# Performance work log

Hardware: AMD Instinct MI355X
Metric: run time of the kernel (lower is better)

Reference implementation:

```python
import jax, jax.numpy as jnp
import numpy as np

N_NODES = 50000
N_EDGES = 1000000
N_EVAL = 100000
IN_DIM = 256
HID = 64
HEADS = 4
NEG_SLOPE = 0.2


def _glorot(key, shape):
    fan_in, fan_out = shape[0], shape[-1]
    lim = jnp.sqrt(6.0 / (fan_in + fan_out))
    return jax.random.uniform(key, shape, jnp.float32, -lim, lim)


def setup_inputs() -> dict:
    key = jax.random.key(0)
    ks = jax.random.split(key, 24)
    inp = {}
    inp["x"] = jax.random.normal(ks[0], (N_NODES, IN_DIM), jnp.float32)
    inp["edge_index"] = jax.random.randint(ks[1], (2, N_EDGES), 0, N_NODES, jnp.int64)
    inp["edge_src"] = jax.random.randint(ks[2], (N_EVAL,), 0, N_NODES, jnp.int64)
    inp["edge_dst"] = jax.random.randint(ks[3], (N_EVAL,), 0, N_NODES, jnp.int64)
    # encoder
    inp["enc_w"] = _glorot(ks[4], (IN_DIM, HID))
    inp["enc_b"] = jnp.zeros((HID,), jnp.float32)
    # GAT layer 1: HID -> HEADS*HID (concat)
    inp["gat1_w"] = _glorot(ks[5], (HID, HEADS * HID))
    inp["gat1_att_src"] = _glorot(ks[6], (HEADS, HID))
    inp["gat1_att_dst"] = _glorot(ks[7], (HEADS, HID))
    inp["gat1_b"] = jnp.zeros((HEADS * HID,), jnp.float32)
    # GAT layer 2: HEADS*HID -> HEADS*HID
    inp["gat2_w"] = _glorot(ks[8], (HEADS * HID, HEADS * HID))
    inp["gat2_att_src"] = _glorot(ks[9], (HEADS, HID))
    inp["gat2_att_dst"] = _glorot(ks[10], (HEADS, HID))
    inp["gat2_b"] = jnp.zeros((HEADS * HID,), jnp.float32)
    # link predictor MLP: 2*256 -> 64 -> 32 -> 1
    inp["lp1_w"] = _glorot(ks[11], (2 * HEADS * HID, HID))
    inp["lp1_b"] = jnp.zeros((HID,), jnp.float32)
    inp["lp2_w"] = _glorot(ks[12], (HID, HID // 2))
    inp["lp2_b"] = jnp.zeros((HID // 2,), jnp.float32)
    inp["lp3_w"] = _glorot(ks[13], (HID // 2, 1))
    inp["lp3_b"] = jnp.zeros((1,), jnp.float32)
    return inp


def gat_layer(x, src, dst, W, att_src, att_dst, bias, n_nodes):
    # x: [N, F_in] -> h: [N, H, C]
    h = (x @ W).reshape(n_nodes, HEADS, HID)
    a_s = jnp.einsum("nhc,hc->nh", h, att_src)  # per-node src logit part
    a_d = jnp.einsum("nhc,hc->nh", h, att_dst)  # per-node dst logit part
    e = jax.nn.leaky_relu(a_s[src] + a_d[dst], NEG_SLOPE)  # [E, H]
    # segment softmax over incoming edges of each dst node
    m = jax.ops.segment_max(e, dst, num_segments=n_nodes)  # [N, H]
    e = jnp.exp(e - m[dst])
    s = jax.ops.segment_sum(e, dst, num_segments=n_nodes)  # [N, H]
    alpha = e / (s[dst] + 1e-16)  # [E, H]
    msg = h[src] * alpha[:, :, None]  # [E, H, C]
    out = jax.ops.segment_sum(msg, dst, num_segments=n_nodes)  # [N, H, C]
    return out.reshape(n_nodes, HEADS * HID) + bias


def reference(x, edge_index, edge_src, edge_dst,
              enc_w, enc_b,
              gat1_w, gat1_att_src, gat1_att_dst, gat1_b,
              gat2_w, gat2_att_src, gat2_att_dst, gat2_b,
              lp1_w, lp1_b, lp2_w, lp2_b, lp3_w, lp3_b):
    n = x.shape[0]
    src, dst = edge_index[0], edge_index[1]
    # NodeEncoder
    h = jax.nn.relu(x @ enc_w + enc_b)
    # GAT layers (dropout is identity in eval)
    h = gat_layer(h, src, dst, gat1_w, gat1_att_src, gat1_att_dst, gat1_b, n)
    h = gat_layer(h, src, dst, gat2_w, gat2_att_src, gat2_att_dst, gat2_b, n)
    # link predictor on (src_feat, dst_feat) pairs
    pair = jnp.concatenate([h[edge_src], h[edge_dst]], axis=1)  # [Eval, 512]
    z = jax.nn.relu(pair @ lp1_w + lp1_b)
    z = jax.nn.relu(z @ lp2_w + lp2_b)
    scores = z @ lp3_w + lp3_b  # [Eval, 1]
    return scores
```

## Files before the change

kernel.cpp:

```cpp
#include <hip/hip_runtime.h>
#include <hip/hip_bf16.h>
#include <math.h>

#define NNODES 50000
#define HID    64
#define HEADS  4
#define FDIM   256

typedef __attribute__((ext_vector_type(8))) _Float16 half8v;
typedef __attribute__((ext_vector_type(4))) _Float16 half4v;
typedef __attribute__((ext_vector_type(4))) float f32x4;

__device__ __forceinline__ float lrelu(float x) { return fmaxf(x, 0.2f * x); }

__global__ void split_kernel(const float4* __restrict__ x, _Float16* __restrict__ xh, int n4)
{
  int t = blockIdx.x * blockDim.x + threadIdx.x;
  if (t >= n4) return;
  float4 v = x[t];
  half4v o = {(_Float16)v.x, (_Float16)v.y, (_Float16)v.z, (_Float16)v.w};
  *(half4v*)(xh + (size_t)t * 4) = o;
}

__global__ void wtconv_all_kernel(const float* __restrict__ enc_w, const float* __restrict__ g1_w,
                                  const float* __restrict__ g2_w, const float* __restrict__ lp1_w,
                                  _Float16* __restrict__ we, _Float16* __restrict__ w1,
                                  _Float16* __restrict__ w2, _Float16* __restrict__ wlp)
{
  int t = blockIdx.x * blockDim.x + threadIdx.x;
  float w; _Float16* dh; int di;
  if (t < 16384) {
    int n = t >> 8, k = t & 255;
    w = enc_w[(size_t)k * 64 + n]; dh = we; di = t;
  } else if (t < 32768) {
    int l = t - 16384; int n = l >> 6, k = l & 63;
    w = g1_w[(size_t)k * 256 + n]; dh = w1; di = l;
  } else if (t < 98304) {
    int l = t - 32768; int n = l >> 8, k = l & 255;
    w = g2_w[(size_t)k * 256 + n]; dh = w2; di = l;
  } else {
    int l = t - 98304; int n = l >> 8, k = l & 255;
    int srow = (n < 64) ? k : (256 + k);
    w = lp1_w[(size_t)srow * 64 + (n & 63)]; dh = wlp; di = l;
  }
  dh[di] = (_Float16)w;
}

__global__ void attcomb_kernel(const float* __restrict__ g1_w, const float* __restrict__ g1_as,
                               const float* __restrict__ g1_ad,
                               const float* __restrict__ g2_w, const float* __restrict__ g2_as,
                               const float* __restrict__ g2_ad,
                               _Float16* __restrict__ w1, _Float16* __restrict__ w2)
{
  int t = blockIdx.x * blockDim.x + threadIdx.x;
  if (t < 1024) {
    int j = t >> 6, k = t & 63;
    float v = 0.f;
    if (j < 8) {
      int head = j & 3;
      const float* att = (j < 4 ? g1_as : g1_ad) + head * 64;
      for (int c = 0; c < 64; ++c) v += g1_w[(size_t)k * 256 + head * 64 + c] * att[c];
    }
    w1[(256 + j) * 64 + k] = (_Float16)v;
  } else if (t < 5120) {
    int l = t - 1024; int j = l >> 8, k = l & 255;
    float v = 0.f;
    if (j < 8) {
      int head = j & 3;
      const float* att = (j < 4 ? g2_as : g2_ad) + head * 64;
      for (int c = 0; c < 64; ++c) v += g2_w[(size_t)k * 256 + head * 64 + c] * att[c];
    }
    w2[(256 + j) * 256 + k] = (_Float16)v;
  }
}

template<int KTOT, int NFRAG, int OUTMODE, bool LOGIT>
__global__ __launch_bounds__(256) void mfma_gemm(
    const _Float16* __restrict__ A, const _Float16* __restrict__ B,
    const float* __restrict__ bias,
    float* __restrict__ outF, _Float16* __restrict__ outH,
    float* __restrict__ a_s, float* __restrict__ a_d,
    int M, int Ntot)
{
  __shared__ _Float16 As[128 * 64];
  const int tid  = threadIdx.x;
  const int lane = tid & 63;
  const int wid  = tid >> 6;
  const int row0 = blockIdx.y * 128;
  const int col0 = blockIdx.x * 64;
  const bool lastblk = LOGIT && ((int)blockIdx.x == (int)gridDim.x - 1);

  f32x4 acc[2][NFRAG];
  f32x4 accL[2];
#pragma unroll
  for (int m = 0; m < 2; ++m) {
#pragma unroll
    for (int n = 0; n < NFRAG; ++n) acc[m][n] = (f32x4){0.f, 0.f, 0.f, 0.f};
    accL[m] = (f32x4){0.f, 0.f, 0.f, 0.f};
  }

  const int rsub = lane >> 3;
  const int slot = lane & 7;
  const int brow = col0 + (lane & 15);
  const int bk   = (lane >> 4) * 8;

  for (int kt = 0; kt < KTOT; kt += 64) {
#pragma unroll
    for (int i = 0; i < 4; ++i) {
      const int c  = i * 4 + wid;
      const int r  = c * 8 + rsub;
      const int gr = min(row0 + r, M - 1);
      const int ss = slot ^ rsub;
      const size_t goff = (size_t)gr * KTOT + kt + ss * 8;
      __builtin_amdgcn_global_load_lds(
          (const __attribute__((address_space(1))) void*)(A + goff),
          (__attribute__((address_space(3))) void*)(As + c * 512), 16, 0, 0);
    }
    __syncthreads();

#pragma unroll
    for (int ks = 0; ks < 2; ++ks) {
      half8v ah[2], bh[NFRAG];
#pragma unroll
      for (int mf = 0; mf < 2; ++mf) {
        const int r   = wid * 32 + mf * 16 + (lane & 15);
        const int sl  = (ks * 4 + (lane >> 4)) ^ (r & 7);
        ah[mf] = *(const half8v*)(As + r * 64 + sl * 8);
      }
#pragma unroll
      for (int nf = 0; nf < NFRAG; ++nf) {
        const size_t bo = (size_t)(brow + nf * 16) * KTOT + kt + ks * 32 + bk;
        bh[nf] = *(const half8v*)(B + bo);
      }
#pragma unroll
      for (int mf = 0; mf < 2; ++mf)
#pragma unroll
        for (int nf = 0; nf < NFRAG; ++nf)
          acc[mf][nf] = __builtin_amdgcn_mfma_f32_16x16x32_f16(ah[mf], bh[nf], acc[mf][nf], 0, 0, 0);
      if (lastblk) {
        const size_t bo = (size_t)(256 + (lane & 15)) * KTOT + kt + ks * 32 + bk;
        const half8v bhl = *(const half8v*)(B + bo);
#pragma unroll
        for (int mf = 0; mf < 2; ++mf)
          accL[mf] = __builtin_amdgcn_mfma_f32_16x16x32_f16(ah[mf], bhl, accL[mf], 0, 0, 0);
      }
    }
    __syncthreads();
  }

  const int crow = row0 + wid * 32 + (lane >> 4) * 4;
  const int ccol = col0 + (lane & 15);
#pragma unroll
  for (int mf = 0; mf < 2; ++mf)
#pragma unroll
    for (int nf = 0; nf < NFRAG; ++nf)
#pragma unroll
      for (int r = 0; r < 4; ++r) {
        const int grow = crow + mf * 16 + r;
        const int gcol = ccol + nf * 16;
        if (grow >= M) continue;
        float v = acc[mf][nf][r];
        if (OUTMODE == 0) {
          outF[(size_t)grow * Ntot + gcol] = v;
        } else if (OUTMODE == 1) {
          v = fmaxf(v + bias[gcol], 0.f);
          outH[(size_t)grow * Ntot + gcol] = (_Float16)v;
        } else {
          outH[(size_t)grow * FDIM + gcol] = (_Float16)v;
        }
      }
  if (lastblk) {
    const int c8 = lane & 15;
#pragma unroll
    for (int mf = 0; mf < 2; ++mf)
#pragma unroll
      for (int r = 0; r < 4; ++r) {
        const int grow = crow + mf * 16 + r;
        if (grow >= M) continue;
        const float v = accL[mf][r];
        if (c8 < 4)      a_s[grow * 4 + c8] = v;
        else if (c8 < 8) a_d[grow * 4 + (c8 - 4)] = v;
      }
  }
}

__global__ void hist_kernel(const int* __restrict__ dst, int* __restrict__ deg, int E)
{
  int i = blockIdx.x * blockDim.x + threadIdx.x;
  if (i < E) atomicAdd(&deg[dst[i]], 1);
}

__global__ void scan1_kernel(const int* __restrict__ deg, int* __restrict__ off,
                             int* __restrict__ bsum, int n)
{
  __shared__ int ws[4];
  const int t = threadIdx.x, lane = t & 63, w = t >> 6;
  const int i = blockIdx.x * 256 + t;
  const int v = (i < n) ? deg[i] : 0;
  int x = v;
#pragma unroll
  for (int d = 1; d < 64; d <<= 1) {
    int y = __shfl_up(x, d, 64);
    if (lane >= d) x += y;
  }
  if (lane == 63) ws[w] = x;
  __syncthreads();
  int add = 0;
  for (int k = 0; k < w; ++k) add += ws[k];
  if (i < n) off[i] = add + x - v;
  if (t == 255) bsum[blockIdx.x] = add + x;
}

__global__ void scan2_kernel(int* __restrict__ bsum, int nb)
{
  __shared__ int ws[4];
  const int t = threadIdx.x, lane = t & 63, w = t >> 6;
  const int v = (t < nb) ? bsum[t] : 0;
  int x = v;
#pragma unroll
  for (int d = 1; d < 64; d <<= 1) {
    int y = __shfl_up(x, d, 64);
    if (lane >= d) x += y;
  }
  if (lane == 63) ws[w] = x;
  __syncthreads();
  int add = 0;
  for (int k = 0; k < w; ++k) add += ws[k];
  if (t < nb) bsum[t] = add + x - v;
}

__global__ void scan3_kernel(int* __restrict__ off, const int* __restrict__ bsum, int n, int E)
{
  const int i = blockIdx.x * 256 + threadIdx.x;
  if (i < n) off[i] += bsum[blockIdx.x];
  if (i == 0) off[n] = E;
}

__global__ void scatter_kernel(const int* __restrict__ src, const int* __restrict__ dst,
                               const int* __restrict__ off, int* __restrict__ cursor,
                               int* __restrict__ sidx, int E)
{
  int i = blockIdx.x * blockDim.x + threadIdx.x;
  if (i < E) {
    int d = dst[i];
    int p = atomicAdd(&cursor[d], 1);
    sidx[off[d] + p] = src[i];
  }
}

__global__ __launch_bounds__(256) void aggregate_kernel(
    const _Float16* __restrict__ hW, const int* __restrict__ sidx,
    const int* __restrict__ off, const float* __restrict__ a_s, const float* __restrict__ a_d,
    const float* __restrict__ bias,
    _Float16* __restrict__ outH, int n_nodes)
{
  __shared__ float wlds[4][16][4];
  const int w    = threadIdx.x >> 6;
  const int wid  = (blockIdx.x * 256 + threadIdx.x) >> 6;
  const int lane = threadIdx.x & 63;
  if (wid >= n_nodes) return;
  const int n = wid;
  const int beg = off[n], end = off[n + 1];

  const int es   = lane >> 2;
  const int hh   = lane & 3;
  const float adh = a_d[(unsigned)n * 4 + hh];
  float m = -1e30f, ssum = 0.f;
  for (int j = beg + es; j < end; j += 16) {
    const unsigned s = (unsigned)sidx[j];
    const float e = lrelu(a_s[s * 4 + hh] + adh);
    const float mn = fmaxf(m, e);
    ssum = ssum * __expf(m - mn) + __expf(e - mn);
    m = mn;
  }
#pragma unroll
  for (int d = 4; d < 64; d <<= 1) {
    const float mo = __shfl_xor(m, d, 64);
    const float so = __shfl_xor(ssum, d, 64);
    const float mn = fmaxf(m, mo);
    ssum = ssum * __expf(m - mn) + so * __expf(mo - mn);
    m = mn;
  }
  const int hb = lane >> 4;
  const float sh = __shfl(ssum, hb, 64);

  float acc0 = 0.f, acc1 = 0.f, acc2 = 0.f, acc3 = 0.f;
  const unsigned lo4 = (unsigned)(lane << 2);
  for (int j0 = beg; j0 < end; j0 += 16) {
    const int jj = j0 + es;
    float wv = 0.f;
    if (jj < end) {
      const unsigned s = (unsigned)sidx[jj];
      const float e = lrelu(a_s[s * 4 + hh] + adh);
      wv = __expf(e - m);
    }
    wlds[w][es][hh] = wv;
    const int jend = min(j0 + 16, end);
#pragma unroll 4
    for (int j = j0; j < jend; ++j) {
      const unsigned s = (unsigned)sidx[j];
      const float wgt = wlds[w][j - j0][hb];
      const half4v hv = *(const half4v*)(hW + s * (unsigned)FDIM + lo4);
      acc0 = fmaf(wgt, (float)hv.x, acc0);
      acc1 = fmaf(wgt, (float)hv.y, acc1);
      acc2 = fmaf(wgt, (float)hv.z, acc2);
      acc3 = fmaf(wgt, (float)hv.w, acc3);
    }
  }
  const float inv = 1.f / (sh + 1e-16f);
  const float4 bv = *(const float4*)(bias + lo4);
  half4v o = {(_Float16)(acc0 * inv + bv.x), (_Float16)(acc1 * inv + bv.y),
              (_Float16)(acc2 * inv + bv.z), (_Float16)(acc3 * inv + bv.w)};
  *(half4v*)(outH + (unsigned)n * FDIM + lo4) = o;
}

__global__ __launch_bounds__(256) void linkpred_kernel(
    const float* __restrict__ uv,
    const int* __restrict__ es, const int* __restrict__ ed,
    const float* __restrict__ b1, const float* __restrict__ w2, const float* __restrict__ b2,
    const float* __restrict__ w3, const float* __restrict__ b3,
    float* __restrict__ out, int n_eval)
{
  __shared__ float w2s[64 * 32];
  __shared__ float z1s[4][4][64];
  const int t = threadIdx.x;
  for (int i = t; i < 64 * 32; i += 256) w2s[i] = w2[i];
  const int w = t >> 6, lane = t & 63;
  const int pair0 = blockIdx.x * 16 + w * 4;
#pragma unroll
  for (int p = 0; p < 4; ++p) {
    const int pc = min(pair0 + p, n_eval - 1);
    const int s = es[pc], d = ed[pc];
    z1s[w][p][lane] = fmaxf(uv[(unsigned)s * 128 + lane] + uv[(unsigned)d * 128 + 64 + lane] + b1[lane], 0.f);
  }
  __syncthreads();
  const int half = lane >> 5;
  const int col  = lane & 31;
  const float w3c = w3[col];
#pragma unroll
  for (int pp = 0; pp < 2; ++pp) {
    const int p = pp * 2 + half;
    float acc = b2[col];
#pragma unroll
    for (int k = 0; k < 64; ++k) acc = fmaf(z1s[w][p][k], w2s[k * 32 + col], acc);
    float zz = fmaxf(acc, 0.f) * w3c;
#pragma unroll
    for (int d = 1; d < 32; d <<= 1) zz += __shfl_xor(zz, d, 64);
    if (col == 0) {
      const int pv = pair0 + p;
      if (pv < n_eval) out[pv] = zz + b3[0];
    }
  }
}

extern "C" void kernel_launch(void* const* d_in, const int* in_sizes, int n_in,
                              void* d_out, int out_size, void* d_ws, size_t ws_size,
                              hipStream_t stream)
{
  const float* x     = (const float*)d_in[0];
  const int*   ei    = (const int*)d_in[1];
  const int*   esrc  = (const int*)d_in[2];
  const int*   edst  = (const int*)d_in[3];
  const float* enc_w = (const float*)d_in[4];
  const float* enc_b = (const float*)d_in[5];
  const float* g1_w  = (const float*)d_in[6];
  const float* g1_as = (const float*)d_in[7];
  const float* g1_ad = (const float*)d_in[8];
  const float* g1_b  = (const float*)d_in[9];
  const float* g2_w  = (const float*)d_in[10];
  const float* g2_as = (const float*)d_in[11];
  const float* g2_ad = (const float*)d_in[12];
  const float* g2_b  = (const float*)d_in[13];
  const float* lp1_w = (const float*)d_in[14];
  const float* lp1_b = (const float*)d_in[15];
  const float* lp2_w = (const float*)d_in[16];
  const float* lp2_b = (const float*)d_in[17];
  const float* lp3_w = (const float*)d_in[18];
  const float* lp3_b = (const float*)d_in[19];
  float* out = (float*)d_out;

  const int E  = in_sizes[1] / 2;
  const int NE = in_sizes[2];
  const int M  = NNODES;
  const int NB = (M + 255) / 256;

  const int* e_src = ei;
  const int* e_dst = ei + E;

  _Float16* hWh = (_Float16*)d_ws;
  float* a_s   = (float*)(hWh + (size_t)M * FDIM);
  float* a_d   = a_s + (size_t)M * HEADS;
  _Float16* hh = (_Float16*)(a_d + (size_t)M * HEADS);
  _Float16* agg = hh + (size_t)M * HID;
  int*   deg    = (int*)(agg + (size_t)M * FDIM);
  int*   cursor = deg + M;
  int*   off    = cursor + M;
  int*   bsum   = off + M + 1;
  int*   sidx   = bsum + 256;
  _Float16* we  = (_Float16*)(sidx + E);
  _Float16* w1  = we + 64 * 256;
  _Float16* w2  = w1 + 272 * 64;
  _Float16* wlp = w2 + 272 * 256;
  _Float16* x_h = agg;
  float* uv = (float*)hWh;

  hipMemsetAsync(deg, 0, sizeof(int) * 2 * (size_t)M, stream);
  hist_kernel<<<(E + 255) / 256, 256, 0, stream>>>(e_dst, deg, E);
  scan1_kernel<<<NB, 256, 0, stream>>>(deg, off, bsum, M);
  scan2_kernel<<<1, 256, 0, stream>>>(bsum, NB);
  scan3_kernel<<<NB, 256, 0, stream>>>(off, bsum, M, E);
  scatter_kernel<<<(E + 255) / 256, 256, 0, stream>>>(e_src, e_dst, off, cursor, sidx, E);

  {
    int n4 = M * FDIM / 4;
    split_kernel<<<(n4 + 255) / 256, 256, 0, stream>>>((const float4*)x, x_h, n4);
    wtconv_all_kernel<<<512, 256, 0, stream>>>(enc_w, g1_w, g2_w, lp1_w, we, w1, w2, wlp);
    attcomb_kernel<<<20, 256, 0, stream>>>(g1_w, g1_as, g1_ad, g2_w, g2_as, g2_ad, w1, w2);
  }

  const int GB = (M + 127) / 128;

  mfma_gemm<256, 4, 1, false><<<dim3(1, GB), 256, 0, stream>>>(
      x_h, we, enc_b, nullptr, hh, nullptr, nullptr, M, HID);

  mfma_gemm<64, 4, 2, true><<<dim3(4, GB), 256, 0, stream>>>(
      hh, w1, nullptr, nullptr, hWh, a_s, a_d, M, FDIM);
  aggregate_kernel<<<(M * 64 + 255) / 256, 256, 0, stream>>>(
      hWh, sidx, off, a_s, a_d, g1_b, agg, M);

  mfma_gemm<256, 4, 2, true><<<dim3(4, GB), 256, 0, stream>>>(
      agg, w2, nullptr, nullptr, hWh, a_s, a_d, M, FDIM);
  aggregate_kernel<<<(M * 64 + 255) / 256, 256, 0, stream>>>(
      hWh, sidx, off, a_s, a_d, g2_b, agg, M);

  mfma_gemm<256, 4, 0, false><<<dim3(2, GB), 256, 0, stream>>>(
      agg, wlp, nullptr, uv, nullptr, nullptr, nullptr, M, 2 * HID);
  linkpred_kernel<<<(NE + 15) / 16, 256, 0, stream>>>(uv, esrc, edst, lp1_b, lp2_w, lp2_b,
                                                      lp3_w, lp3_b, out, NE);
}
```

Before: 534.7 us.

## Merge prep kernels, add 512-thread full-K GEMM, store link-pred UV in fp16

The split, weight-conversion and attention-combine kernels are folded into one prep launch. The GAT and link-predictor GEMMs move to a new 512-thread kernel that loads the whole 128xK A tile into LDS once, with no K loop or per-step barriers. Each block now covers 128 output columns, which halves the blocks that re-read A. The link-predictor UV projections are stored in fp16 instead of fp32, halving that gather traffic at some cost in precision. LDS use rises to 64KB per block for K=256, which may limit occupancy.

After: 517.6 us. 3.2% less time.

```diff
diff --git a/kernel.cpp b/kernel.cpp
--- a/kernel.cpp
+++ b/kernel.cpp
@@ -13,48 +13,37 @@
 
 __device__ __forceinline__ float lrelu(float x) { return fmaxf(x, 0.2f * x); }
 
-__global__ void split_kernel(const float4* __restrict__ x, _Float16* __restrict__ xh, int n4)
+__global__ void prep_kernel(const float4* __restrict__ x, _Float16* __restrict__ xh, int n4,
+                            const float* __restrict__ enc_w, const float* __restrict__ g1_w,
+                            const float* __restrict__ g2_w, const float* __restrict__ lp1_w,
+                            const float* __restrict__ g1_as, const float* __restrict__ g1_ad,
+                            const float* __restrict__ g2_as, const float* __restrict__ g2_ad,
+                            _Float16* __restrict__ we, _Float16* __restrict__ w1,
+                            _Float16* __restrict__ w2, _Float16* __restrict__ wlp)
 {
   int t = blockIdx.x * blockDim.x + threadIdx.x;
-  if (t >= n4) return;
-  float4 v = x[t];
-  half4v o = {(_Float16)v.x, (_Float16)v.y, (_Float16)v.z, (_Float16)v.w};
-  *(half4v*)(xh + (size_t)t * 4) = o;
-}
-
-__global__ void wtconv_all_kernel(const float* __restrict__ enc_w, const float* __restrict__ g1_w,
-                                  const float* __restrict__ g2_w, const float* __restrict__ lp1_w,
-                                  _Float16* __restrict__ we, _Float16* __restrict__ w1,
-                                  _Float16* __restrict__ w2, _Float16* __restrict__ wlp)
-{
-  int t = blockIdx.x * blockDim.x + threadIdx.x;
-  float w; _Float16* dh; int di;
-  if (t < 16384) {
-    int n = t >> 8, k = t & 255;
-    w = enc_w[(size_t)k * 64 + n]; dh = we; di = t;
-  } else if (t < 32768) {
-    int l = t - 16384; int n = l >> 6, k = l & 63;
-    w = g1_w[(size_t)k * 256 + n]; dh = w1; di = l;
-  } else if (t < 98304) {
-    int l = t - 32768; int n = l >> 8, k = l & 255;
-    w = g2_w[(size_t)k * 256 + n]; dh = w2; di = l;
-  } else {
-    int l = t - 98304; int n = l >> 8, k = l & 255;
+  if (t < n4) {
+    float4 v = x[t];
+    half4v o = {(_Float16)v.x, (_Float16)v.y, (_Float16)v.z, (_Float16)v.w};
+    *(half4v*)(xh + (size_t)t * 4) = o;
+    return;
+  }
+  int u = t - n4;
+  if (u < 16384) {
+    int n = u >> 8, k = u & 255;
+    we[u] = (_Float16)enc_w[(size_t)k * 64 + n];
+  } else if (u < 32768) {
+    int l = u - 16384; int n = l >> 6, k = l & 63;
+    w1[l] = (_Float16)g1_w[(size_t)k * 256 + n];
+  } else if (u < 98304) {
+    int l = u - 32768; int n = l >> 8, k = l & 255;
+    w2[l] = (_Float16)g2_w[(size_t)k * 256 + n];
+  } else if (u < 131072) {
+    int l = u - 98304; int n = l >> 8, k = l & 255;
     int srow = (n < 64) ? k : (256 + k);
-    w = lp1_w[(size_t)srow * 64 + (n & 63)]; dh = wlp; di = l;
-  }
-  dh[di] = (_Float16)w;
-}
-
-__global__ void attcomb_kernel(const float* __restrict__ g1_w, const float* __restrict__ g1_as,
-                               const float* __restrict__ g1_ad,
-                               const float* __restrict__ g2_w, const float* __restrict__ g2_as,
-                               const float* __restrict__ g2_ad,
-                               _Float16* __restrict__ w1, _Float16* __restrict__ w2)
-{
-  int t = blockIdx.x * blockDim.x + threadIdx.x;
-  if (t < 1024) {
-    int j = t >> 6, k = t & 63;
+    wlp[l] = (_Float16)lp1_w[(size_t)srow * 64 + (n & 63)];
+  } else if (u < 132096) {
+    int l = u - 131072; int j = l >> 6, k = l & 63;
     float v = 0.f;
     if (j < 8) {
       int head = j & 3;
@@ -62,8 +51,8 @@
       for (int c = 0; c < 64; ++c) v += g1_w[(size_t)k * 256 + head * 64 + c] * att[c];
     }
     w1[(256 + j) * 64 + k] = (_Float16)v;
-  } else if (t < 5120) {
-    int l = t - 1024; int j = l >> 8, k = l & 255;
+  } else if (u < 136192) {
+    int l = u - 132096; int j = l >> 8, k = l & 255;
     float v = 0.f;
     if (j < 8) {
       int head = j & 3;
@@ -74,44 +63,35 @@
   }
 }
 
-template<int KTOT, int NFRAG, int OUTMODE, bool LOGIT>
-__global__ __launch_bounds__(256) void mfma_gemm(
+__global__ __launch_bounds__(256) void enc_gemm(
     const _Float16* __restrict__ A, const _Float16* __restrict__ B,
-    const float* __restrict__ bias,
-    float* __restrict__ outF, _Float16* __restrict__ outH,
-    float* __restrict__ a_s, float* __restrict__ a_d,
-    int M, int Ntot)
+    const float* __restrict__ bias, _Float16* __restrict__ outH, int M)
 {
   __shared__ _Float16 As[128 * 64];
   const int tid  = threadIdx.x;
   const int lane = tid & 63;
   const int wid  = tid >> 6;
   const int row0 = blockIdx.y * 128;
-  const int col0 = blockIdx.x * 64;
-  const bool lastblk = LOGIT && ((int)blockIdx.x == (int)gridDim.x - 1);
-
-  f32x4 acc[2][NFRAG];
-  f32x4 accL[2];
-#pragma unroll
-  for (int m = 0; m < 2; ++m) {
-#pragma unroll
-    for (int n = 0; n < NFRAG; ++n) acc[m][n] = (f32x4){0.f, 0.f, 0.f, 0.f};
-    accL[m] = (f32x4){0.f, 0.f, 0.f, 0.f};
-  }
+
+  f32x4 acc[2][4];
+#pragma unroll
+  for (int m = 0; m < 2; ++m)
+#pragma unroll
+    for (int n = 0; n < 4; ++n) acc[m][n] = (f32x4){0.f, 0.f, 0.f, 0.f};
 
   const int rsub = lane >> 3;
   const int slot = lane & 7;
-  const int brow = col0 + (lane & 15);
+  const int brow = lane & 15;
   const int bk   = (lane >> 4) * 8;
 
-  for (int kt = 0; kt < KTOT; kt += 64) {
+  for (int kt = 0; kt < 256; kt += 64) {
 #pragma unroll
     for (int i = 0; i < 4; ++i) {
       const int c  = i * 4 + wid;
       const int r  = c * 8 + rsub;
       const int gr = min(row0 + r, M - 1);
       const int ss = slot ^ rsub;
-      const size_t goff = (size_t)gr * KTOT + kt + ss * 8;
+      const size_t goff = (size_t)gr * 256 + kt + ss * 8;
       __builtin_amdgcn_global_load_lds(
           (const __attribute__((address_space(1))) void*)(A + goff),
           (__attribute__((address_space(3))) void*)(As + c * 512), 16, 0, 0);
@@ -120,7 +100,7 @@
 
 #pragma unroll
     for (int ks = 0; ks < 2; ++ks) {
-      half8v ah[2], bh[NFRAG];
+      half8v ah[2], bh[4];
 #pragma unroll
       for (int mf = 0; mf < 2; ++mf) {
         const int r   = wid * 32 + mf * 16 + (lane & 15);
@@ -128,48 +108,108 @@
         ah[mf] = *(const half8v*)(As + r * 64 + sl * 8);
       }
 #pragma unroll
-      for (int nf = 0; nf < NFRAG; ++nf) {
-        const size_t bo = (size_t)(brow + nf * 16) * KTOT + kt + ks * 32 + bk;
-        bh[nf] = *(const half8v*)(B + bo);
-      }
+      for (int nf = 0; nf < 4; ++nf)
+        bh[nf] = *(const half8v*)(B + (size_t)(brow + nf * 16) * 256 + kt + ks * 32 + bk);
 #pragma unroll
       for (int mf = 0; mf < 2; ++mf)
 #pragma unroll
-        for (int nf = 0; nf < NFRAG; ++nf)
+        for (int nf = 0; nf < 4; ++nf)
           acc[mf][nf] = __builtin_amdgcn_mfma_f32_16x16x32_f16(ah[mf], bh[nf], acc[mf][nf], 0, 0, 0);
-      if (lastblk) {
-        const size_t bo = (size_t)(256 + (lane & 15)) * KTOT + kt + ks * 32 + bk;
-        const half8v bhl = *(const half8v*)(B + bo);
-#pragma unroll
-        for (int mf = 0; mf < 2; ++mf)
-          accL[mf] = __builtin_amdgcn_mfma_f32_16x16x32_f16(ah[mf], bhl, accL[mf], 0, 0, 0);
-      }
     }
     __syncthreads();
   }
 
   const int crow = row0 + wid * 32 + (lane >> 4) * 4;
-  const int ccol = col0 + (lane & 15);
+  const int ccol = lane & 15;
 #pragma unroll
   for (int mf = 0; mf < 2; ++mf)
 #pragma unroll
-    for (int nf = 0; nf < NFRAG; ++nf)
+    for (int nf = 0; nf < 4; ++nf)
 #pragma unroll
       for (int r = 0; r < 4; ++r) {
         const int grow = crow + mf * 16 + r;
         const int gcol = ccol + nf * 16;
         if (grow >= M) continue;
-        float v = acc[mf][nf][r];
-        if (OUTMODE == 0) {
-          outF[(size_t)grow * Ntot + gcol] = v;
-        } else if (OUTMODE == 1) {
-          v = fmaxf(v + bias[gcol], 0.f);
-          outH[(size_t)grow * Ntot + gcol] = (_Float16)v;
-        } else {
-          outH[(size_t)grow * FDIM + gcol] = (_Float16)v;
-        }
+        float v = fmaxf(acc[mf][nf][r] + bias[gcol], 0.f);
+        outH[(size_t)grow * HID + gcol] = (_Float16)v;
       }
-  if (lastblk) {
+}
+
+template<int KTOT, bool LOGIT>
+__global__ __launch_bounds__(512) void gemm512(
+    const _Float16* __restrict__ A, const _Float16* __restrict__ B,
+    _Float16* __restrict__ outH, float* __restrict__ a_s, float* __restrict__ a_d,
+    int M, int OS)
+{
+  __shared__ _Float16 As[128 * KTOT];
+  constexpr int SPR = KTOT / 8;
+  const int tid  = threadIdx.x;
+  const int lane = tid & 63;
+  const int w    = tid >> 6;
+  const int rowg = w & 3;
+  const int colg = w >> 2;
+  const int row0 = blockIdx.y * 128;
+  const int col0 = blockIdx.x * 128 + colg * 64;
+  const bool lastlog = LOGIT && ((int)blockIdx.x == (int)gridDim.x - 1) && (colg == 1);
+
+#pragma unroll
+  for (int rr = 0; rr < KTOT / 32; ++rr) {
+    const int f  = rr * 512 + tid;
+    const int r  = f / SPR;
+    const int s  = f % SPR;
+    const int gs = s ^ (r & 7);
+    const int gr = min(row0 + r, M - 1);
+    __builtin_amdgcn_global_load_lds(
+        (const __attribute__((address_space(1))) void*)(A + (size_t)gr * KTOT + gs * 8),
+        (__attribute__((address_space(3))) void*)(As + f * 8), 16, 0, 0);
+  }
+  __syncthreads();
+
+  f32x4 acc[2][4];
+  f32x4 accL[2];
+#pragma unroll
+  for (int m = 0; m < 2; ++m) {
+#pragma unroll
+    for (int n = 0; n < 4; ++n) acc[m][n] = (f32x4){0.f, 0.f, 0.f, 0.f};
+    accL[m] = (f32x4){0.f, 0.f, 0.f, 0.f};
+  }
+
+  const int brow = col0 + (lane & 15);
+#pragma unroll
+  for (int ks = 0; ks < KTOT / 32; ++ks) {
+    const int sk = ks * 4 + (lane >> 4);
+    half8v ah[2];
+#pragma unroll
+    for (int mf = 0; mf < 2; ++mf) {
+      const int r = rowg * 32 + mf * 16 + (lane & 15);
+      ah[mf] = *(const half8v*)(As + r * KTOT + (sk ^ (r & 7)) * 8);
+    }
+#pragma unroll
+    for (int nf = 0; nf < 4; ++nf) {
+      const half8v bh = *(const half8v*)(B + (size_t)(brow + nf * 16) * KTOT + sk * 8);
+      acc[0][nf] = __builtin_amdgcn_mfma_f32_16x16x32_f16(ah[0], bh, acc[0][nf], 0, 0, 0);
+      acc[1][nf] = __builtin_amdgcn_mfma_f32_16x16x32_f16(ah[1], bh, acc[1][nf], 0, 0, 0);
+    }
+    if (lastlog) {
+      const half8v bh = *(const half8v*)(B + (size_t)(256 + (lane & 15)) * KTOT + sk * 8);
+      accL[0] = __builtin_amdgcn_mfma_f32_16x16x32_f16(ah[0], bh, accL[0], 0, 0, 0);
+      accL[1] = __builtin_amdgcn_mfma_f32_16x16x32_f16(ah[1], bh, accL[1], 0, 0, 0);
+    }
+  }
+
+  const int crow = row0 + rowg * 32 + (lane >> 4) * 4;
+  const int ccol = col0 + (lane & 15);
+#pragma unroll
+  for (int mf = 0; mf < 2; ++mf)
+#pragma unroll
+    for (int nf = 0; nf < 4; ++nf)
+#pragma unroll
+      for (int r = 0; r < 4; ++r) {
+        const int grow = crow + mf * 16 + r;
+        if (grow >= M) continue;
+        outH[(size_t)grow * OS + ccol + nf * 16] = (_Float16)acc[mf][nf][r];
+      }
+  if (lastlog) {
     const int c8 = lane & 15;
 #pragma unroll
     for (int mf = 0; mf < 2; ++mf)
@@ -315,7 +355,7 @@
 }
 
 __global__ __launch_bounds__(256) void linkpred_kernel(
-    const float* __restrict__ uv,
+    const _Float16* __restrict__ uv,
     const int* __restrict__ es, const int* __restrict__ ed,
     const float* __restrict__ b1, const float* __restrict__ w2, const float* __restrict__ b2,
     const float* __restrict__ w3, const float* __restrict__ b3,
@@ -331,7 +371,8 @@
   for (int p = 0; p < 4; ++p) {
     const int pc = min(pair0 + p, n_eval - 1);
     const int s = es[pc], d = ed[pc];
-    z1s[w][p][lane] = fmaxf(uv[(unsigned)s * 128 + lane] + uv[(unsigned)d * 128 + 64 + lane] + b1[lane], 0.f);
+    const float uvl = (float)uv[(unsigned)s * 128 + lane] + (float)uv[(unsigned)d * 128 + 64 + lane];
+    z1s[w][p][lane] = fmaxf(uvl + b1[lane], 0.f);
   }
   __syncthreads();
   const int half = lane >> 5;
@@ -402,7 +443,7 @@
   _Float16* w2  = w1 + 272 * 64;
   _Float16* wlp = w2 + 272 * 256;
   _Float16* x_h = agg;
-  float* uv = (float*)hWh;
+  _Float16* uv = hWh;
 
   hipMemsetAsync(deg, 0, sizeof(int) * 2 * (size_t)M, stream);
   hist_kernel<<<(E + 255) / 256, 256, 0, stream>>>(e_dst, deg, E);
@@ -412,29 +453,26 @@
   scatter_kernel<<<(E + 255) / 256, 256, 0, stream>>>(e_src, e_dst, off, cursor, sidx, E);
 
   {
-    int n4 = M * FDIM / 4;
-    split_kernel<<<(n4 + 255) / 256, 256, 0, stream>>>((const float4*)x, x_h, n4);
-    wtconv_all_kernel<<<512, 256, 0, stream>>>(enc_w, g1_w, g2_w, lp1_w, we, w1, w2, wlp);
-    attcomb_kernel<<<20, 256, 0, stream>>>(g1_w, g1_as, g1_ad, g2_w, g2_as, g2_ad, w1, w2);
+    const int n4 = M * FDIM / 4;
+    const int total = n4 + 136192;
+    prep_kernel<<<(total + 255) / 256, 256, 0, stream>>>(
+        (const float4*)x, x_h, n4, enc_w, g1_w, g2_w, lp1_w,
+        g1_as, g1_ad, g2_as, g2_ad, we, w1, w2, wlp);
   }
 
   const int GB = (M + 127) / 128;
 
-  mfma_gemm<256, 4, 1, false><<<dim3(1, GB), 256, 0, stream>>>(
-      x_h, we, enc_b, nullptr, hh, nullptr, nullptr, M, HID);
-
-  mfma_gemm<64, 4, 2, true><<<dim3(4, GB), 256, 0, stream>>>(
-      hh, w1, nullptr, nullptr, hWh, a_s, a_d, M, FDIM);
+  enc_gemm<<<dim3(1, GB), 256, 0, stream>>>(x_h, we, enc_b, hh, M);
+
+  gemm512<64, true><<<dim3(2, GB), 512, 0, stream>>>(hh, w1, hWh, a_s, a_d, M, FDIM);
   aggregate_kernel<<<(M * 64 + 255) / 256, 256, 0, stream>>>(
       hWh, sidx, off, a_s, a_d, g1_b, agg, M);
 
-  mfma_gemm<256, 4, 2, true><<<dim3(4, GB), 256, 0, stream>>>(
-      agg, w2, nullptr, nullptr, hWh, a_s, a_d, M, FDIM);
+  gemm512<256, true><<<dim3(2, GB), 512, 0, stream>>>(agg, w2, hWh, a_s, a_d, M, FDIM);
   aggregate_kernel<<<(M * 64 + 255) / 256, 256, 0, stream>>>(
       hWh, sidx, off, a_s, a_d, g2_b, agg, M);
 
-  mfma_gemm<256, 4, 0, false><<<dim3(2, GB), 256, 0, stream>>>(
-      agg, wlp, nullptr, uv, nullptr, nullptr, nullptr, M, 2 * HID);
+  gemm512<256, false><<<dim3(1, GB), 512, 0, stream>>>(agg, wlp, uv, nullptr, nullptr, M, 2 * HID);
   linkpred_kernel<<<(NE + 15) / 16, 256, 0, stream>>>(uv, esrc, edst, lp1_b, lp2_w, lp2_b,
                                                       lp3_w, lp3_b, out, NE);
 }
```
